# Optimization experiments

Hardware: AMD Instinct MI355X
Metric: run time of the kernel (lower is better)

Reference implementation:

```python
import jax, jax.numpy as jnp
import numpy as np

C = 64          # num_channels
NB = 8          # num_bessel
NE = 10         # num_elements
N_NODES = 20000
N_EDGES = 320000

def _silu_norm():
    # e3nn normalize2mom constant for silu: 1/sqrt(E[silu(Z)^2]), Z~N(0,1)
    x, w = np.polynomial.hermite.hermgauss(100)
    z = np.sqrt(2.0) * x
    f = z / (1.0 + np.exp(-z))
    m2 = float(np.sum(w * f * f) / np.sqrt(np.pi))
    return np.float32(1.0 / np.sqrt(m2))

C_SILU = _silu_norm()
SQRT3 = np.float32(np.sqrt(3.0))
SQRT2 = np.float32(np.sqrt(2.0))
INV_SQRT_C = np.float32(1.0 / np.sqrt(C))
INV_SQRT_2C = np.float32(1.0 / np.sqrt(2 * C))
INV_SQRT_3C = np.float32(1.0 / np.sqrt(3 * C))
INV_SQRT_NB = np.float32(1.0 / np.sqrt(NB))
INV_SQRT_64 = np.float32(1.0 / np.sqrt(64.0))


def setup_inputs() -> dict:
    key = jax.random.key(0)
    ks = jax.random.split(key, 22)
    n = lambda k, s: jax.random.normal(k, s, dtype=jnp.float32)
    return {
        "node_feats": n(ks[0], (N_NODES, 4 * C)),
        "edge_feats": jax.random.uniform(ks[1], (N_EDGES, NB), dtype=jnp.float32),
        "edge_attrs": n(ks[2], (N_EDGES, 4)),
        "iedges": jax.random.randint(ks[3], (N_EDGES,), 0, N_NODES),
        "jedges": jax.random.randint(ks[4], (N_EDGES,), 0, N_NODES),
        "atomic_numbers": jax.random.randint(ks[5], (N_NODES,), 0, NE),
        "Wup0": n(ks[6], (C, C)), "Wup1": n(ks[7], (C, C)),
        "Wm1": n(ks[8], (NB, 64)), "Wm2": n(ks[9], (64, 64)),
        "Wm3": n(ks[10], (64, 64)), "Wm4": n(ks[11], (64, 5 * C)),
        "Wl0": n(ks[12], (2 * C, C)), "Wl1": n(ks[13], (3 * C, C)),
        "Ws0c1": n(ks[14], (NE, 1, C)), "Ws0c2": n(ks[15], (NE, 2, C)),
        "Ws0c3": n(ks[16], (NE, 2, C)),
        "Ws1c1": n(ks[17], (NE, 1, C)), "Ws1c2": n(ks[18], (NE, 1, C)),
        "Ws1c3": n(ks[19], (NE, 2, C)),
        "Wp0": n(ks[20], (C, C)), "Wp1": n(ks[21], (C, C)),
    }


def reference(node_feats, edge_feats, edge_attrs, iedges, jedges, atomic_numbers,
              Wup0, Wup1, Wm1, Wm2, Wm3, Wm4, Wl0, Wl1,
              Ws0c1, Ws0c2, Ws0c3, Ws1c1, Ws1c2, Ws1c3, Wp0, Wp1):
    Nn = node_feats.shape[0]
    # split irreps: C scalars (0e) then C vectors (1e), channel-major layout
    s = node_feats[:, :C]                       # (N, C)
    v = node_feats[:, C:].reshape(Nn, C, 3)     # (N, C, 3)

    # linear_up: per-l channel mixing, fan-in normalized (e3nn o3.Linear)
    s = (s @ Wup0) * INV_SQRT_C
    v = jnp.einsum('ncm,ck->nkm', v, Wup1) * INV_SQRT_C

    # conv_tp_weights: e3nn FullyConnectedNet [8,64,64,64,5C] with silu
    h = jax.nn.silu(edge_feats @ (Wm1 * INV_SQRT_NB)) * C_SILU
    h = jax.nn.silu(h @ (Wm2 * INV_SQRT_64)) * C_SILU
    h = jax.nn.silu(h @ (Wm3 * INV_SQRT_64)) * C_SILU
    tpw = h @ (Wm4 * INV_SQRT_64)               # (E, 5C)

    # gather sender node features per edge
    xs = s[iedges]                              # (E, C)
    xv = v[iedges]                              # (E, C, 3)
    eas = edge_attrs[:, 0:1]                    # (E, 1) scalar edge attr
    eav = edge_attrs[:, 1:4]                    # (E, 3) vector edge attr

    # 5 uvu CG paths (component-normalized e3nn TensorProduct):
    wa, wb = tpw[:, 0:C], tpw[:, C:2 * C]
    wc, wd, we = tpw[:, 2 * C:3 * C], tpw[:, 3 * C:4 * C], tpw[:, 4 * C:5 * C]
    m0 = wa * xs * eas                                              # 0e x 0e -> 0e
    m1 = wb * jnp.einsum('ecm,em->ec', xv, eav) / SQRT3             # 1e x 1e -> 0e
    m2 = (wc * xs)[:, :, None] * eav[:, None, :]                    # 0e x 1e -> 1e
    m3 = (wd * eas)[:, :, None] * xv                                # 1e x 0e -> 1e
    m4 = we[:, :, None] * jnp.cross(xv, eav[:, None, :]) / SQRT2    # 1e x 1e -> 1e

    # scatter-sum messages to receiver nodes
    msg_s = jax.ops.segment_sum(jnp.concatenate([m0, m1], axis=1), jedges, num_segments=Nn)        # (N, 2C)
    msg_v = jax.ops.segment_sum(jnp.concatenate([m2, m3, m4], axis=1), jedges, num_segments=Nn)    # (N, 3C, 3)

    # linear: middle irreps (2C x 0e + 3C x 1e) -> C x (0e + 1e)
    s2 = (msg_s @ Wl0) * INV_SQRT_2C            # (N, C)
    v2 = jnp.einsum('ncm,ck->nkm', msg_v, Wl1) * INV_SQRT_3C  # (N, C, 3)

    # symmetric (ACE/MACE) contraction, correlation=3, element-dependent weights
    w01 = Ws0c1[atomic_numbers, 0]              # (N, C)
    w02 = Ws0c2[atomic_numbers]                 # (N, 2, C)
    w03 = Ws0c3[atomic_numbers]                 # (N, 2, C)
    w11 = Ws1c1[atomic_numbers, 0]
    w12 = Ws1c2[atomic_numbers, 0]
    w13 = Ws1c3[atomic_numbers]
    vv = jnp.sum(v2 * v2, axis=-1)              # (N, C) = |v|^2 per channel
    out_s = (w01 * s2 + w02[:, 0] * s2 * s2 + w02[:, 1] * vv / SQRT3
             + w03[:, 0] * s2 * s2 * s2 + w03[:, 1] * s2 * vv / SQRT3)
    coef_v = w11 + w12 * s2 + w13[:, 0] * s2 * s2 + w13[:, 1] * vv / SQRT3
    out_v = coef_v[:, :, None] * v2             # (N, C, 3)

    # linearproduct
    so = (out_s @ Wp0) * INV_SQRT_C
    vo = jnp.einsum('ncm,ck->nkm', out_v, Wp1) * INV_SQRT_C
    return jnp.concatenate([so, vo.reshape(Nn, 3 * C)], axis=1)   # (N, 4C)
```

## Files before the change

### kernel.cpp

```cpp
#include <hip/hip_runtime.h>


typedef unsigned short u16;
typedef unsigned int u32;
typedef __attribute__((ext_vector_type(8))) short bf16x8;
typedef __attribute__((ext_vector_type(4))) float f32x4;

#define CW_UP0 0
#define CW_UP1 4096
#define CW_M1  8192
#define CW_M2  8704
#define CW_M3  12800
#define CW_M4  16896
#define CW_L0  37376
#define CW_L1  45568
#define CW_P0  57856
#define CW_P1  61952
#define CW_S01 66048
#define CW_S02 66688
#define CW_S03 67968
#define CW_S11 69248
#define CW_S12 69888
#define CW_S13 70528
#define CW_TOTAL 71808

#define C_SILU     1.6765224f
#define INV_SQRT3  0.57735027f
#define INV_SQRT2  0.70710678f
#define SC_L1      0.35355339f
#define SC_L234    0.125f

#define HS16 72
#define NFRAG   60

__device__ __forceinline__ float b2f(u16 u) {
  union { u32 i; float f; } x; x.i = ((u32)u) << 16; return x.f;
}
__device__ __forceinline__ u16 f2b(float f) {
  union { float f; u32 i; } x; x.f = f;
  u32 i = x.i;
  u32 r = (i + 0x7fffu + ((i >> 16) & 1u)) >> 16;
  return (u16)r;
}
__device__ __forceinline__ float ldf(const void* p, size_t i, int f32) {
  return f32 ? ((const float*)p)[i] : b2f(((const u16*)p)[i]);
}
__device__ __forceinline__ float silu_n(float x) {
  return C_SILU * x / (1.0f + __expf(-x));
}

__global__ void k_detect(const void* nf, int* flag) {
  __shared__ int cnt;
  if (threadIdx.x == 0) cnt = 0;
  __syncthreads();
  const u16* p = (const u16*)nf;
  int wild = 0;
  for (int i = threadIdx.x; i < 4096; i += 256) {
    float ax = fabsf(b2f(p[i]));
    if (!(ax <= 1e10f) || (ax != 0.f && ax < 1e-10f)) wild++;
  }
  atomicAdd(&cnt, wild);
  __syncthreads();
  if (threadIdx.x == 0) *flag = (cnt > 100) ? 1 : 0;
}

struct WPtrs { const void* p[16]; };

__global__ __launch_bounds__(256) void k_front(
    WPtrs wp, float* __restrict__ cw, u16* __restrict__ bwH,
    u16* __restrict__ bwL, const int* __restrict__ je, int* __restrict__ deg,
    const void* __restrict__ nf, float* __restrict__ sup,
    float* __restrict__ vup, int nN, int nE, int nb0,
    const int* __restrict__ flagp) {
  __shared__ float row[4][256];
  const int f32 = *flagp;
  int bid = blockIdx.x, tid = threadIdx.x;

  if (bid < 281) {
    const int   sizes[16]  = {4096,4096,512,4096,4096,20480,8192,12288,4096,
                              4096,640,1280,1280,640,640,1280};
    const float scales[16] = {0.125f,0.125f,0.35355339f,0.125f,0.125f,0.125f,
                              0.08838835f,0.07216878f,0.125f,0.125f,
                              1.f,1.f,1.f,1.f,1.f,1.f};
    int gid = bid * 256 + tid;
    if (gid >= CW_TOTAL) return;
    int off = gid, seg = 0;
    while (off >= sizes[seg]) { off -= sizes[seg]; seg++; }
    cw[gid] = ldf(wp.p[seg], off, f32) * scales[seg];
  } else if (bid < 401) {
    int gid = (bid - 281) * 256 + tid;
    int f = gid >> 9, idx = gid & 511;
    int l = idx >> 3, j = idx & 7;
    int q = l >> 4, col16 = l & 15;
    float v = 0.f;
    if (f < 4) {
      int k = q * 8 + j, n = f * 16 + col16;
      if (k < 8) v = ldf(wp.p[2], (size_t)k * 64 + n, f32);
    } else if (f < 20) {
      const void* w = (f < 12) ? wp.p[3] : wp.p[4];
      int t = (f < 12) ? f - 4 : f - 12;
      int n = (t >> 1) * 16 + col16, ks = t & 1;
      int k = ks * 32 + q * 8 + j;
      v = ldf(w, (size_t)k * 64 + n, f32);
    } else {
      int t = f - 20;
      int n = (t >> 1) * 16 + col16, ks = t & 1;
      int k = ks * 32 + q * 8 + j;
      v = ldf(wp.p[5], (size_t)k * 320 + n, f32);
    }
    u16 hi = f2b(v);
    u16 lo = f2b(v - b2f(hi));
    size_t o = (size_t)f * 512 + (size_t)l * 8 + j;
    bwH[o] = hi;
    bwL[o] = lo;
  } else if (bid < nb0) {
    int e = (bid - 401) * 256 + tid;
    if (e < nE) atomicAdd(&deg[je[e]], 1);
  } else {
    int w = tid >> 6, l = tid & 63;
    int n = (bid - nb0) * 4 + w;
    bool valid = n < nN;
    int nn = valid ? n : 0;
#pragma unroll
    for (int t = 0; t < 4; t++)
      row[w][t * 64 + l] = ldf(nf, (size_t)nn * 256 + t * 64 + l, f32);
    __syncthreads();
    float sacc = 0.f, v0 = 0.f, v1 = 0.f, v2 = 0.f;
#pragma unroll 8
    for (int c = 0; c < 64; c++) {
      float w0 = ldf(wp.p[0], (size_t)c * 64 + l, f32);
      float w1 = ldf(wp.p[1], (size_t)c * 64 + l, f32);
      sacc += row[w][c] * w0;
      v0 += row[w][64 + c * 3 + 0] * w1;
      v1 += row[w][64 + c * 3 + 1] * w1;
      v2 += row[w][64 + c * 3 + 2] * w1;
    }
    if (valid) {
      sup[(size_t)n * 64 + l] = sacc * 0.125f;
      vup[((size_t)n * 3 + 0) * 64 + l] = v0 * 0.125f;
      vup[((size_t)n * 3 + 1) * 64 + l] = v1 * 0.125f;
      vup[((size_t)n * 3 + 2) * 64 + l] = v2 * 0.125f;
    }
  }
}

__global__ __launch_bounds__(256) void k_scan(const int* __restrict__ deg,
                                              int* __restrict__ offs,
                                              int* __restrict__ cursor, int nN) {
  __shared__ int part[256];
  int t = threadIdx.x;
  int per = (nN + 255) / 256;
  int lo = t * per, hi = (t + 1) * per; if (hi > nN) hi = nN;
  int s = 0;
  for (int i = lo; i < hi; i++) s += deg[i];
  part[t] = s;
  __syncthreads();
  if (t == 0) {
    int run = 0;
    for (int i = 0; i < 256; i++) { int v = part[i]; part[i] = run; run += v; }
    offs[nN] = run;
  }
  __syncthreads();
  int run = part[t];
  for (int i = lo; i < hi; i++) {
    offs[i] = run; cursor[i] = run; run += deg[i];
  }
}

__global__ __launch_bounds__(256) void k_scatter2(
    const int* __restrict__ je, const int* __restrict__ ie,
    const void* __restrict__ ea, const void* __restrict__ ef,
    int* __restrict__ cursor, int* __restrict__ iSlot,
    float4* __restrict__ eaSlot, float4* __restrict__ efSlot, int nE,
    const int* __restrict__ flagp) {
  const int f32 = *flagp;
  int e = blockIdx.x * 256 + threadIdx.x;
  if (e >= nE) return;
  int pos = atomicAdd(&cursor[je[e]], 1);
  iSlot[pos] = ie[e];
  float4 av;
  float4 f0, f1;
  if (f32) {
    av = ((const float4*)ea)[e];
    f0 = ((const float4*)ef)[(size_t)e * 2];
    f1 = ((const float4*)ef)[(size_t)e * 2 + 1];
  } else {
    uint2 r = ((const uint2*)ea)[e];
    av = make_float4(b2f(r.x & 0xffff), b2f(r.x >> 16),
                     b2f(r.y & 0xffff), b2f(r.y >> 16));
    uint4 u = ((const uint4*)ef)[e];
    f0 = make_float4(b2f(u.x & 0xffff), b2f(u.x >> 16),
                     b2f(u.y & 0xffff), b2f(u.y >> 16));
    f1 = make_float4(b2f(u.z & 0xffff), b2f(u.z >> 16),
                     b2f(u.w & 0xffff), b2f(u.w >> 16));
  }
  eaSlot[pos] = av;
  efSlot[(size_t)pos * 2] = f0;
  efSlot[(size_t)pos * 2 + 1] = f1;
}

__global__ __launch_bounds__(192) void k_mlp4(
    const float4* __restrict__ efSlot, const int* __restrict__ offs,
    const u16* __restrict__ bwH, const u16* __restrict__ bwL,
    u16* __restrict__ tpw, int gn0, int gn1, int capEff) {
  __shared__ u16 H[3][64 * HS16];
  int tid = threadIdx.x;
  int w = tid >> 6, l = tid & 63;
  int m = l & 15, q = l >> 4;
  int base = offs[gn0];
  int cnt = offs[gn1] - base;
  int lim = cnt < capEff ? cnt : capEff;
  int tb = (blockIdx.x * 3 + w) * 64;
  if (tb >= lim) return;
  u16* Hw = H[w];

  bf16x8 zero8 = {0,0,0,0,0,0,0,0};
  bf16x8 A1h[4], A1l[4];
#pragma unroll
  for (int t = 0; t < 4; t++) { A1h[t] = zero8; A1l[t] = zero8; }
  if (q == 0) {
#pragma unroll
    for (int t = 0; t < 4; t++) {
      int s = tb + t * 16 + m; if (s > lim - 1) s = lim - 1;
      float4 q0 = efSlot[(size_t)s * 2], q1 = efSlot[(size_t)s * 2 + 1];
      float v[8] = {q0.x, q0.y, q0.z, q0.w, q1.x, q1.y, q1.z, q1.w};
      bf16x8 hi, lo;
#pragma unroll
      for (int j = 0; j < 8; j++) {
        u16 h = f2b(v[j]);
        hi[j] = (short)h;
        lo[j] = (short)f2b(v[j] - b2f(h));
      }
      A1h[t] = hi; A1l[t] = lo;
    }
  }
#pragma unroll
  for (int n = 0; n < 4; n++) {
    bf16x8 Bh = *(const bf16x8*)(bwH + (size_t)n * 512 + (size_t)l * 8);
    bf16x8 Bl = *(const bf16x8*)(bwL + (size_t)n * 512 + (size_t)l * 8);
#pragma unroll
    for (int t = 0; t < 4; t++) {
      f32x4 c = (f32x4){0.f, 0.f, 0.f, 0.f};
      c = __builtin_amdgcn_mfma_f32_16x16x32_bf16(A1h[t], Bh, c, 0, 0, 0);
      c = __builtin_amdgcn_mfma_f32_16x16x32_bf16(A1l[t], Bh, c, 0, 0, 0);
      c = __builtin_amdgcn_mfma_f32_16x16x32_bf16(A1h[t], Bl, c, 0, 0, 0);
#pragma unroll
      for (int r = 0; r < 4; r++)
        Hw[(t * 16 + q * 4 + r) * HS16 + n * 16 + m] =
            f2b(silu_n(c[r] * SC_L1));
    }
  }

#pragma unroll
  for (int layer = 0; layer < 2; layer++) {
    int fragBase = 4 + layer * 8;
    bf16x8 Ah[2][4];
#pragma unroll
    for (int ks = 0; ks < 2; ks++)
#pragma unroll
      for (int t = 0; t < 4; t++)
        Ah[ks][t] = *(const bf16x8*)(Hw + (t * 16 + m) * HS16 + ks * 32 + q * 8);
#pragma unroll
    for (int n = 0; n < 4; n++) {
      bf16x8 B0h = *(const bf16x8*)(bwH + (size_t)(fragBase + n * 2 + 0) * 512 +
                                    (size_t)l * 8);
      bf16x8 B0l = *(const bf16x8*)(bwL + (size_t)(fragBase + n * 2 + 0) * 512 +
                                    (size_t)l * 8);
      bf16x8 B1h = *(const bf16x8*)(bwH + (size_t)(fragBase + n * 2 + 1) * 512 +
                                    (size_t)l * 8);
      bf16x8 B1l = *(const bf16x8*)(bwL + (size_t)(fragBase + n * 2 + 1) * 512 +
                                    (size_t)l * 8);
#pragma unroll
      for (int t = 0; t < 4; t++) {
        f32x4 c = (f32x4){0.f, 0.f, 0.f, 0.f};
        c = __builtin_amdgcn_mfma_f32_16x16x32_bf16(Ah[0][t], B0h, c, 0, 0, 0);
        c = __builtin_amdgcn_mfma_f32_16x16x32_bf16(Ah[0][t], B0l, c, 0, 0, 0);
        c = __builtin_amdgcn_mfma_f32_16x16x32_bf16(Ah[1][t], B1h, c, 0, 0, 0);
        c = __builtin_amdgcn_mfma_f32_16x16x32_bf16(Ah[1][t], B1l, c, 0, 0, 0);
#pragma unroll
        for (int r = 0; r < 4; r++)
          Hw[(t * 16 + q * 4 + r) * HS16 + n * 16 + m] =
              f2b(silu_n(c[r] * SC_L234));
      }
    }
  }

  {
    bf16x8 Ah[2][4];
#pragma unroll
    for (int ks = 0; ks < 2; ks++)
#pragma unroll
      for (int t = 0; t < 4; t++)
        Ah[ks][t] = *(const bf16x8*)(Hw + (t * 16 + m) * HS16 + ks * 32 + q * 8);
    for (int n = 0; n < 20; n++) {
      bf16x8 B0h = *(const bf16x8*)(bwH + (size_t)(20 + n * 2 + 0) * 512 +
                                    (size_t)l * 8);
      bf16x8 B0l = *(const bf16x8*)(bwL + (size_t)(20 + n * 2 + 0) * 512 +
                                    (size_t)l * 8);
      bf16x8 B1h = *(const bf16x8*)(bwH + (size_t)(20 + n * 2 + 1) * 512 +
                                    (size_t)l * 8);
      bf16x8 B1l = *(const bf16x8*)(bwL + (size_t)(20 + n * 2 + 1) * 512 +
                                    (size_t)l * 8);
#pragma unroll
      for (int t = 0; t < 4; t++) {
        f32x4 c = (f32x4){0.f, 0.f, 0.f, 0.f};
        c = __builtin_amdgcn_mfma_f32_16x16x32_bf16(Ah[0][t], B0h, c, 0, 0, 0);
        c = __builtin_amdgcn_mfma_f32_16x16x32_bf16(Ah[0][t], B0l, c, 0, 0, 0);
        c = __builtin_amdgcn_mfma_f32_16x16x32_bf16(Ah[1][t], B1h, c, 0, 0, 0);
        c = __builtin_amdgcn_mfma_f32_16x16x32_bf16(Ah[1][t], B1l, c, 0, 0, 0);
#pragma unroll
        for (int r = 0; r < 4; r++) {
          int srow = tb + t * 16 + q * 4 + r;
          if (srow < lim)
            tpw[(size_t)srow * 320 + n * 16 + m] = f2b(c[r] * SC_L234);
        }
      }
    }
  }
}

__global__ __launch_bounds__(256) void k_gather5(
    const int* __restrict__ iSlot, const float4* __restrict__ eaSlot,
    const int* __restrict__ offs, const float* __restrict__ sup,
    const float* __restrict__ vup, const int* __restrict__ an,
    const float* __restrict__ cw, const u16* __restrict__ tpw,
    void* __restrict__ out, int gn0, int gn1, int capEff,
    const int* __restrict__ flagp) {
  __shared__ float B[4][960];
  const int f32 = *flagp;
  int w = threadIdx.x >> 6, l = threadIdx.x & 63;
  int n = gn0 + blockIdx.x * 4 + w;
  bool valid = n < gn1;
  int nn = valid ? n : gn0;
  int gbase = offs[gn0];
  int start = offs[nn];
  int deg = offs[nn + 1] - start;
  int avail = capEff - (start - gbase);
  int dmax = deg < avail ? deg : avail;
  if (dmax < 0) dmax = 0;

  float as0 = 0.f, as1 = 0.f;
  float av[9];
#pragma unroll
  for (int m = 0; m < 9; m++) av[m] = 0.f;

  for (int c0 = 0; c0 < dmax; c0 += 64) {
    int rem = dmax - c0;
    int cend = rem < 64 ? rem : 64;
    int iA = 0;
    float4 eaA = make_float4(0.f, 0.f, 0.f, 0.f);
    if (l < cend) {
      iA = iSlot[start + c0 + l];
      eaA = eaSlot[start + c0 + l];
    }
    for (int qq = 0; qq < cend; qq++) {
      int i = __shfl(iA, qq);
      float eas = __shfl(eaA.x, qq);
      float ev0 = __shfl(eaA.y, qq);
      float ev1 = __shfl(eaA.z, qq);
      float ev2 = __shfl(eaA.w, qq);
      const u16* tp = tpw + (size_t)(start - gbase + c0 + qq) * 320;
      float wa  = b2f(tp[l]);
      float wbv = b2f(tp[64 + l]);
      float wc  = b2f(tp[128 + l]);
      float wd  = b2f(tp[192 + l]);
      float we_ = b2f(tp[256 + l]);
      float xs  = sup[(size_t)i * 64 + l];
      float xv0 = vup[((size_t)i * 3 + 0) * 64 + l];
      float xv1 = vup[((size_t)i * 3 + 1) * 64 + l];
      float xv2 = vup[((size_t)i * 3 + 2) * 64 + l];
      float dot = xv0 * ev0 + xv1 * ev1 + xv2 * ev2;
      as0 += wa * xs * eas;
      as1 += wbv * dot * INV_SQRT3;
      float wcxs = wc * xs;
      float wde  = wd * eas;
      float wef  = we_ * INV_SQRT2;
      av[0] += wcxs * ev0; av[1] += wcxs * ev1; av[2] += wcxs * ev2;
      av[3] += wde * xv0;  av[4] += wde * xv1;  av[5] += wde * xv2;
      av[6] += wef * (xv1 * ev2 - xv2 * ev1);
      av[7] += wef * (xv2 * ev0 - xv0 * ev2);
      av[8] += wef * (xv0 * ev1 - xv1 * ev0);
    }
  }

  float* Bb = B[w];
  Bb[l] = as0;
  Bb[64 + l] = as1;
#pragma unroll
  for (int m = 0; m < 3; m++) {
    Bb[128 + l * 3 + m] = av[m];
    Bb[320 + l * 3 + m] = av[3 + m];
    Bb[512 + l * 3 + m] = av[6 + m];
  }
  __syncthreads();

  float s2 = 0.f;
#pragma unroll 8
  for (int c = 0; c < 128; c++) s2 += Bb[c] * cw[CW_L0 + c * 64 + l];
  float v20 = 0.f, v21 = 0.f, v22 = 0.f;
#pragma unroll 8
  for (int c = 0; c < 192; c++) {
    float wk = cw[CW_L1 + c * 64 + l];
    v20 += Bb[128 + c * 3 + 0] * wk;
    v21 += Bb[128 + c * 3 + 1] * wk;
    v22 += Bb[128 + c * 3 + 2] * wk;
  }
  int a = an[nn];
  float w01  = cw[CW_S01 + a * 64 + l];
  float w02a = cw[CW_S02 + a * 128 + l];
  float w02b = cw[CW_S02 + a * 128 + 64 + l];
  float w03a = cw[CW_S03 + a * 128 + l];
  float w03b = cw[CW_S03 + a * 128 + 64 + l];
  float w11  = cw[CW_S11 + a * 64 + l];
  float w12  = cw[CW_S12 + a * 64 + l];
  float w13a = cw[CW_S13 + a * 128 + l];
  float w13b = cw[CW_S13 + a * 128 + 64 + l];

  float vv = v20 * v20 + v21 * v21 + v22 * v22;
  float s2sq = s2 * s2;
  float vvs = vv * INV_SQRT3;
  float outs = w01 * s2 + w02a * s2sq + w02b * vvs + w03a * s2sq * s2 +
               w03b * s2 * vvs;
  float coef = w11 + w12 * s2 + w13a * s2sq + w13b * vvs;

  __syncthreads();
  Bb[704 + l] = outs;
  Bb[768 + l * 3 + 0] = coef * v20;
  Bb[768 + l * 3 + 1] = coef * v21;
  Bb[768 + l * 3 + 2] = coef * v22;
  __syncthreads();

  float so = 0.f, vo0 = 0.f, vo1 = 0.f, vo2 = 0.f;
#pragma unroll 8
  for (int c = 0; c < 64; c++) {
    float w0 = cw[CW_P0 + c * 64 + l];
    float w1 = cw[CW_P1 + c * 64 + l];
    so  += Bb[704 + c] * w0;
    vo0 += Bb[768 + c * 3 + 0] * w1;
    vo1 += Bb[768 + c * 3 + 1] * w1;
    vo2 += Bb[768 + c * 3 + 2] * w1;
  }
  if (valid) {
    size_t basep = (size_t)n * 256;
    if (f32) {
      float* o = (float*)out;
      o[basep + l] = so;
      o[basep + 64 + l * 3 + 0] = vo0;
      o[basep + 64 + l * 3 + 1] = vo1;
      o[basep + 64 + l * 3 + 2] = vo2;
    } else {
      u16* o = (u16*)out;
      o[basep + l] = f2b(so);
      o[basep + 64 + l * 3 + 0] = f2b(vo0);
      o[basep + 64 + l * 3 + 1] = f2b(vo1);
      o[basep + 64 + l * 3 + 2] = f2b(vo2);
    }
  }
}

extern "C" void kernel_launch(void* const* d_in, const int* in_sizes, int n_in,
                              void* d_out, int out_size, void* d_ws,
                              size_t ws_size, hipStream_t stream) {
  const void* nf = d_in[0];
  const void* ef = d_in[1];
  const void* ea = d_in[2];
  const int* ie = (const int*)d_in[3];
  const int* je = (const int*)d_in[4];
  const int* an = (const int*)d_in[5];
  int nN = in_sizes[0] / 256;
  int nE = in_sizes[3];

  size_t intCnt = (size_t)3 * nN + 1 + nE;
  intCnt = (intCnt + 3) & ~(size_t)3;
  int* deg    = (int*)d_ws;
  int* offs   = deg + nN;
  int* cursor = offs + nN + 1;
  int* iSlot  = cursor + nN;
  float* cw   = (float*)d_ws + intCnt;
  float* sup  = cw + CW_TOTAL;
  float* vup  = sup + (size_t)nN * 64;
  int* flag   = (int*)(vup + (size_t)nN * 192);

  size_t eaByte = (intCnt + CW_TOTAL + (size_t)nN * 256 + 1) * 4;
  eaByte = (eaByte + 15) & ~(size_t)15;
  float4* eaSlot = (float4*)((char*)d_ws + eaByte);
  float4* efSlot = eaSlot + nE;
  size_t bwByte = eaByte + (size_t)nE * 16 + (size_t)nE * 32;
  u16* bwH = (u16*)((char*)d_ws + bwByte);
  u16* bwL = bwH + (size_t)NFRAG * 512;
  size_t tpwByte = bwByte + (size_t)NFRAG * 512 * 2 * 2;
  tpwByte = (tpwByte + 15) & ~(size_t)15;
  u16* tpw = (u16*)((char*)d_ws + tpwByte);
  size_t capE = (ws_size > tpwByte) ? (ws_size - tpwByte) / 640 : 0;

  int G = 64;
  int nodesPer = (nN + 63) / 64;
  for (int g = 1; g <= 64; g++) {
    int npg = (nN + g - 1) / g;
    size_t worst = (size_t)npg * nE / nN + 6000;
    if (worst <= capE) { G = g; nodesPer = npg; break; }
  }
  int capEff = (int)((size_t)nodesPer * nE / nN + 6000);
  if ((size_t)capEff > capE) capEff = (int)capE;

  k_detect<<<1, 256, 0, stream>>>(nf, flag);
  hipMemsetAsync(deg, 0, (size_t)nN * sizeof(int), stream);

  WPtrs wp;
  const int widx[16] = {6, 7, 8, 9, 10, 11, 12, 13, 20, 21,
                        14, 15, 16, 17, 18, 19};
  for (int i = 0; i < 16; i++) wp.p[i] = d_in[widx[i]];

  int histNB = (nE + 255) / 256;
  int nb0 = 401 + histNB;
  int nupNB = (nN + 3) / 4;
  k_front<<<nb0 + nupNB, 256, 0, stream>>>(wp, cw, bwH, bwL, je, deg, nf,
                                           sup, vup, nN, nE, nb0, flag);
  k_scan<<<1, 256, 0, stream>>>(deg, offs, cursor, nN);
  k_scatter2<<<(nE + 255) / 256, 256, 0, stream>>>(je, ie, ea, ef, cursor,
                                                   iSlot, eaSlot, efSlot, nE,
                                                   flag);

  for (int g = 0; g < G; g++) {
    int gn0 = g * nodesPer;
    if (gn0 >= nN) break;
    int gn1 = gn0 + nodesPer; if (gn1 > nN) gn1 = nN;
    int mlpBlocks = (capEff + 191) / 192;
    k_mlp4<<<mlpBlocks, 192, 0, stream>>>(efSlot, offs, bwH, bwL, tpw,
                                          gn0, gn1, capEff);
    int gBlocks = (gn1 - gn0 + 3) / 4;
    k_gather5<<<gBlocks, 256, 0, stream>>>(iSlot, eaSlot, offs, sup, vup, an,
                                           cw, tpw, d_out, gn0, gn1, capEff,
                                           flag);
  }
}
```

Measured before the change: 481.4 us.

## Move per-node linear and product layers into a batched MFMA post kernel

The gather kernel no longer applies the Wl0/Wl1 linears, the symmetric contraction and the Wp0/Wp1 product per node with scalar FMA loops. It now writes the aggregated messages to workspace buffers. A new k_post kernel handles tiles of 64 nodes and runs those matmuls on bf16 MFMA, using a hi/lo split with three products to keep near-fp32 accuracy. The front kernel pre-packs the extra weight fragments. The trade is extra global traffic to write and re-read the message buffers. The mlp kernel's edge-feature read also now offsets by the group base, which matters when there is more than one node group.

New measurement: 585.5 us. 1.22x slower.

```diff
diff --git a/kernel.cpp b/kernel.cpp
--- a/kernel.cpp
+++ b/kernel.cpp
@@ -31,7 +31,11 @@
 #define SC_L234    0.125f
 
 #define HS16 72
-#define NFRAG   60
+#define NFRAG 116
+#define FW0 60
+#define FW1 76
+#define FP0 100
+#define FP1 108
 
 __device__ __forceinline__ float b2f(u16 u) {
   union { u32 i; float f; } x; x.i = ((u32)u) << 16; return x.f;
@@ -87,7 +91,7 @@
     int off = gid, seg = 0;
     while (off >= sizes[seg]) { off -= sizes[seg]; seg++; }
     cw[gid] = ldf(wp.p[seg], off, f32) * scales[seg];
-  } else if (bid < 401) {
+  } else if (bid < 513) {
     int gid = (bid - 281) * 256 + tid;
     int f = gid >> 9, idx = gid & 511;
     int l = idx >> 3, j = idx & 7;
@@ -102,11 +106,27 @@
       int n = (t >> 1) * 16 + col16, ks = t & 1;
       int k = ks * 32 + q * 8 + j;
       v = ldf(w, (size_t)k * 64 + n, f32);
-    } else {
+    } else if (f < 60) {
       int t = f - 20;
       int n = (t >> 1) * 16 + col16, ks = t & 1;
       int k = ks * 32 + q * 8 + j;
       v = ldf(wp.p[5], (size_t)k * 320 + n, f32);
+    } else if (f < 76) {
+      int t = f - FW0, ks = t >> 2, n = t & 3;
+      int k = ks * 32 + q * 8 + j;
+      v = ldf(wp.p[6], (size_t)k * 64 + n * 16 + col16, f32) * 0.08838835f;
+    } else if (f < 100) {
+      int t = f - FW1, ks = t >> 2, n = t & 3;
+      int k = ks * 32 + q * 8 + j;
+      v = ldf(wp.p[7], (size_t)k * 64 + n * 16 + col16, f32) * 0.07216878f;
+    } else if (f < 108) {
+      int t = f - FP0, ks = t >> 2, n = t & 3;
+      int k = ks * 32 + q * 8 + j;
+      v = ldf(wp.p[8], (size_t)k * 64 + n * 16 + col16, f32) * 0.125f;
+    } else {
+      int t = f - FP1, ks = t >> 2, n = t & 3;
+      int k = ks * 32 + q * 8 + j;
+      v = ldf(wp.p[9], (size_t)k * 64 + n * 16 + col16, f32) * 0.125f;
     }
     u16 hi = f2b(v);
     u16 lo = f2b(v - b2f(hi));
@@ -114,7 +134,7 @@
     bwH[o] = hi;
     bwL[o] = lo;
   } else if (bid < nb0) {
-    int e = (bid - 401) * 256 + tid;
+    int e = (bid - 513) * 256 + tid;
     if (e < nE) atomicAdd(&deg[je[e]], 1);
   } else {
     int w = tid >> 6, l = tid & 63;
@@ -222,7 +242,8 @@
 #pragma unroll
     for (int t = 0; t < 4; t++) {
       int s = tb + t * 16 + m; if (s > lim - 1) s = lim - 1;
-      float4 q0 = efSlot[(size_t)s * 2], q1 = efSlot[(size_t)s * 2 + 1];
+      float4 q0 = efSlot[((size_t)(base + s)) * 2];
+      float4 q1 = efSlot[((size_t)(base + s)) * 2 + 1];
       float v[8] = {q0.x, q0.y, q0.z, q0.w, q1.x, q1.y, q1.z, q1.w};
       bf16x8 hi, lo;
 #pragma unroll
@@ -319,22 +340,18 @@
   }
 }
 
-__global__ __launch_bounds__(256) void k_gather5(
+__global__ __launch_bounds__(256) void k_gather6(
     const int* __restrict__ iSlot, const float4* __restrict__ eaSlot,
     const int* __restrict__ offs, const float* __restrict__ sup,
-    const float* __restrict__ vup, const int* __restrict__ an,
-    const float* __restrict__ cw, const u16* __restrict__ tpw,
-    void* __restrict__ out, int gn0, int gn1, int capEff,
-    const int* __restrict__ flagp) {
-  __shared__ float B[4][960];
-  const int f32 = *flagp;
+    const float* __restrict__ vup, const u16* __restrict__ tpw,
+    float* __restrict__ msgS, float* __restrict__ msgV,
+    int gn0, int gn1, int capEff) {
   int w = threadIdx.x >> 6, l = threadIdx.x & 63;
   int n = gn0 + blockIdx.x * 4 + w;
-  bool valid = n < gn1;
-  int nn = valid ? n : gn0;
+  if (n >= gn1) return;
   int gbase = offs[gn0];
-  int start = offs[nn];
-  int deg = offs[nn + 1] - start;
+  int start = offs[n];
+  int deg = offs[n + 1] - start;
   int avail = capEff - (start - gbase);
   int dmax = deg < avail ? deg : avail;
   if (dmax < 0) dmax = 0;
@@ -383,79 +400,172 @@
     }
   }
 
-  float* Bb = B[w];
-  Bb[l] = as0;
-  Bb[64 + l] = as1;
-#pragma unroll
-  for (int m = 0; m < 3; m++) {
-    Bb[128 + l * 3 + m] = av[m];
-    Bb[320 + l * 3 + m] = av[3 + m];
-    Bb[512 + l * 3 + m] = av[6 + m];
-  }
-  __syncthreads();
-
-  float s2 = 0.f;
-#pragma unroll 8
-  for (int c = 0; c < 128; c++) s2 += Bb[c] * cw[CW_L0 + c * 64 + l];
-  float v20 = 0.f, v21 = 0.f, v22 = 0.f;
-#pragma unroll 8
-  for (int c = 0; c < 192; c++) {
-    float wk = cw[CW_L1 + c * 64 + l];
-    v20 += Bb[128 + c * 3 + 0] * wk;
-    v21 += Bb[128 + c * 3 + 1] * wk;
-    v22 += Bb[128 + c * 3 + 2] * wk;
-  }
-  int a = an[nn];
-  float w01  = cw[CW_S01 + a * 64 + l];
-  float w02a = cw[CW_S02 + a * 128 + l];
-  float w02b = cw[CW_S02 + a * 128 + 64 + l];
-  float w03a = cw[CW_S03 + a * 128 + l];
-  float w03b = cw[CW_S03 + a * 128 + 64 + l];
-  float w11  = cw[CW_S11 + a * 64 + l];
-  float w12  = cw[CW_S12 + a * 64 + l];
-  float w13a = cw[CW_S13 + a * 128 + l];
-  float w13b = cw[CW_S13 + a * 128 + 64 + l];
-
-  float vv = v20 * v20 + v21 * v21 + v22 * v22;
-  float s2sq = s2 * s2;
-  float vvs = vv * INV_SQRT3;
-  float outs = w01 * s2 + w02a * s2sq + w02b * vvs + w03a * s2sq * s2 +
-               w03b * s2 * vvs;
-  float coef = w11 + w12 * s2 + w13a * s2sq + w13b * vvs;
-
-  __syncthreads();
-  Bb[704 + l] = outs;
-  Bb[768 + l * 3 + 0] = coef * v20;
-  Bb[768 + l * 3 + 1] = coef * v21;
-  Bb[768 + l * 3 + 2] = coef * v22;
-  __syncthreads();
-
-  float so = 0.f, vo0 = 0.f, vo1 = 0.f, vo2 = 0.f;
-#pragma unroll 8
-  for (int c = 0; c < 64; c++) {
-    float w0 = cw[CW_P0 + c * 64 + l];
-    float w1 = cw[CW_P1 + c * 64 + l];
-    so  += Bb[704 + c] * w0;
-    vo0 += Bb[768 + c * 3 + 0] * w1;
-    vo1 += Bb[768 + c * 3 + 1] * w1;
-    vo2 += Bb[768 + c * 3 + 2] * w1;
-  }
-  if (valid) {
-    size_t basep = (size_t)n * 256;
-    if (f32) {
-      float* o = (float*)out;
-      o[basep + l] = so;
-      o[basep + 64 + l * 3 + 0] = vo0;
-      o[basep + 64 + l * 3 + 1] = vo1;
-      o[basep + 64 + l * 3 + 2] = vo2;
-    } else {
-      u16* o = (u16*)out;
-      o[basep + l] = f2b(so);
-      o[basep + 64 + l * 3 + 0] = f2b(vo0);
-      o[basep + 64 + l * 3 + 1] = f2b(vo1);
-      o[basep + 64 + l * 3 + 2] = f2b(vo2);
-    }
-  }
+  msgS[(size_t)n * 128 + l] = as0;
+  msgS[(size_t)n * 128 + 64 + l] = as1;
+#pragma unroll
+  for (int c = 0; c < 3; c++) {
+    msgV[(size_t)n * 576 + c * 192 + l]       = av[c];
+    msgV[(size_t)n * 576 + c * 192 + 64 + l]  = av[3 + c];
+    msgV[(size_t)n * 576 + c * 192 + 128 + l] = av[6 + c];
+  }
+}
+
+#define POST_G2(SRC, FB, STORE_S, COMP)                                        \
+  {                                                                            \
+    __syncthreads();                                                           \
+    _Pragma("unroll")                                                          \
+    for (int t = 0; t < 4; t++)                                                \
+      _Pragma("unroll")                                                        \
+      for (int r = 0; r < 4; r++)                                              \
+        T[t * 16 + q * 4 + r][w * 16 + m] = SRC[t][r];                         \
+    __syncthreads();                                                           \
+    f32x4 d[4];                                                                \
+    _Pragma("unroll")                                                          \
+    for (int t = 0; t < 4; t++) d[t] = (f32x4){0.f, 0.f, 0.f, 0.f};            \
+    _Pragma("unroll")                                                          \
+    for (int ks = 0; ks < 2; ks++) {                                           \
+      bf16x8 Bh = *(const bf16x8*)(bwH + (size_t)(FB + ks * 4 + w) * 512 +     \
+                                   (size_t)l * 8);                             \
+      bf16x8 Bl = *(const bf16x8*)(bwL + (size_t)(FB + ks * 4 + w) * 512 +     \
+                                   (size_t)l * 8);                             \
+      _Pragma("unroll")                                                        \
+      for (int t = 0; t < 4; t++) {                                            \
+        bf16x8 Ah, Al;                                                         \
+        _Pragma("unroll")                                                      \
+        for (int j = 0; j < 8; j++) {                                          \
+          float vx = T[t * 16 + m][ks * 32 + q * 8 + j];                       \
+          u16 h = f2b(vx);                                                     \
+          Ah[j] = (short)h;                                                    \
+          Al[j] = (short)f2b(vx - b2f(h));                                     \
+        }                                                                      \
+        d[t] = __builtin_amdgcn_mfma_f32_16x16x32_bf16(Ah, Bh, d[t], 0, 0, 0); \
+        d[t] = __builtin_amdgcn_mfma_f32_16x16x32_bf16(Al, Bh, d[t], 0, 0, 0); \
+        d[t] = __builtin_amdgcn_mfma_f32_16x16x32_bf16(Ah, Bl, d[t], 0, 0, 0); \
+      }                                                                        \
+    }                                                                          \
+    _Pragma("unroll")                                                          \
+    for (int t = 0; t < 4; t++)                                                \
+      _Pragma("unroll")                                                        \
+      for (int r = 0; r < 4; r++) {                                            \
+        int node = n0 + t * 16 + q * 4 + r;                                    \
+        if (node < nN) {                                                       \
+          int ch = w * 16 + m;                                                 \
+          size_t basep = (size_t)node * 256;                                   \
+          size_t oidx = STORE_S ? (basep + ch) : (basep + 64 + ch * 3 + COMP); \
+          if (f32) ((float*)out)[oidx] = d[t][r];                              \
+          else ((u16*)out)[oidx] = f2b(d[t][r]);                               \
+        }                                                                      \
+      }                                                                        \
+  }
+
+__global__ __launch_bounds__(256) void k_post(
+    const float* __restrict__ msgS, const float* __restrict__ msgV,
+    const int* __restrict__ an, const float* __restrict__ cw,
+    const u16* __restrict__ bwH, const u16* __restrict__ bwL,
+    void* __restrict__ out, int nN, const int* __restrict__ flagp) {
+  __shared__ float T[64][69];
+  const int f32 = *flagp;
+  int tid = threadIdx.x;
+  int w = tid >> 6, l = tid & 63;
+  int m = l & 15, q = l >> 4;
+  int n0 = blockIdx.x * 64;
+
+  f32x4 s2[4];
+#pragma unroll
+  for (int t = 0; t < 4; t++) s2[t] = (f32x4){0.f, 0.f, 0.f, 0.f};
+#pragma unroll
+  for (int ks = 0; ks < 4; ks++) {
+    bf16x8 Bh = *(const bf16x8*)(bwH + (size_t)(FW0 + ks * 4 + w) * 512 +
+                                 (size_t)l * 8);
+    bf16x8 Bl = *(const bf16x8*)(bwL + (size_t)(FW0 + ks * 4 + w) * 512 +
+                                 (size_t)l * 8);
+#pragma unroll
+    for (int t = 0; t < 4; t++) {
+      int row = n0 + t * 16 + m; if (row > nN - 1) row = nN - 1;
+      const float* ap = msgS + (size_t)row * 128 + ks * 32 + q * 8;
+      bf16x8 Ah, Al;
+#pragma unroll
+      for (int j = 0; j < 8; j++) {
+        float vx = ap[j];
+        u16 h = f2b(vx);
+        Ah[j] = (short)h;
+        Al[j] = (short)f2b(vx - b2f(h));
+      }
+      s2[t] = __builtin_amdgcn_mfma_f32_16x16x32_bf16(Ah, Bh, s2[t], 0, 0, 0);
+      s2[t] = __builtin_amdgcn_mfma_f32_16x16x32_bf16(Al, Bh, s2[t], 0, 0, 0);
+      s2[t] = __builtin_amdgcn_mfma_f32_16x16x32_bf16(Ah, Bl, s2[t], 0, 0, 0);
+    }
+  }
+
+  f32x4 v2[3][4];
+#pragma unroll
+  for (int c = 0; c < 3; c++)
+#pragma unroll
+    for (int t = 0; t < 4; t++) v2[c][t] = (f32x4){0.f, 0.f, 0.f, 0.f};
+#pragma unroll
+  for (int ks = 0; ks < 6; ks++) {
+    bf16x8 Bh = *(const bf16x8*)(bwH + (size_t)(FW1 + ks * 4 + w) * 512 +
+                                 (size_t)l * 8);
+    bf16x8 Bl = *(const bf16x8*)(bwL + (size_t)(FW1 + ks * 4 + w) * 512 +
+                                 (size_t)l * 8);
+#pragma unroll
+    for (int c = 0; c < 3; c++)
+#pragma unroll
+      for (int t = 0; t < 4; t++) {
+        int row = n0 + t * 16 + m; if (row > nN - 1) row = nN - 1;
+        const float* ap = msgV + (size_t)row * 576 + c * 192 + ks * 32 + q * 8;
+        bf16x8 Ah, Al;
+#pragma unroll
+        for (int j = 0; j < 8; j++) {
+          float vx = ap[j];
+          u16 h = f2b(vx);
+          Ah[j] = (short)h;
+          Al[j] = (short)f2b(vx - b2f(h));
+        }
+        v2[c][t] = __builtin_amdgcn_mfma_f32_16x16x32_bf16(Ah, Bh, v2[c][t], 0, 0, 0);
+        v2[c][t] = __builtin_amdgcn_mfma_f32_16x16x32_bf16(Al, Bh, v2[c][t], 0, 0, 0);
+        v2[c][t] = __builtin_amdgcn_mfma_f32_16x16x32_bf16(Ah, Bl, v2[c][t], 0, 0, 0);
+      }
+  }
+
+  f32x4 os[4];
+  f32x4 ov[3][4];
+#pragma unroll
+  for (int t = 0; t < 4; t++) {
+#pragma unroll
+    for (int r = 0; r < 4; r++) {
+      int node = n0 + t * 16 + q * 4 + r;
+      int nc = node > nN - 1 ? nN - 1 : node;
+      int a = an[nc];
+      int ch = w * 16 + m;
+      float s2v = s2[t][r];
+      float va = v2[0][t][r], vb = v2[1][t][r], vc = v2[2][t][r];
+      float vv = va * va + vb * vb + vc * vc;
+      float w01  = cw[CW_S01 + a * 64 + ch];
+      float w02a = cw[CW_S02 + a * 128 + ch];
+      float w02b = cw[CW_S02 + a * 128 + 64 + ch];
+      float w03a = cw[CW_S03 + a * 128 + ch];
+      float w03b = cw[CW_S03 + a * 128 + 64 + ch];
+      float w11  = cw[CW_S11 + a * 64 + ch];
+      float w12  = cw[CW_S12 + a * 64 + ch];
+      float w13a = cw[CW_S13 + a * 128 + ch];
+      float w13b = cw[CW_S13 + a * 128 + 64 + ch];
+      float s2sq = s2v * s2v;
+      float vvs = vv * INV_SQRT3;
+      float outs = w01 * s2v + w02a * s2sq + w02b * vvs + w03a * s2sq * s2v +
+                   w03b * s2v * vvs;
+      float coef = w11 + w12 * s2v + w13a * s2sq + w13b * vvs;
+      os[t][r] = outs;
+      ov[0][t][r] = coef * va;
+      ov[1][t][r] = coef * vb;
+      ov[2][t][r] = coef * vc;
+    }
+  }
+
+  POST_G2(os, FP0, 1, 0)
+  POST_G2(ov[0], FP1, 0, 0)
+  POST_G2(ov[1], FP1, 0, 1)
+  POST_G2(ov[2], FP1, 0, 2)
 }
 
 extern "C" void kernel_launch(void* const* d_in, const int* in_sizes, int n_in,
@@ -480,8 +590,10 @@
   float* sup  = cw + CW_TOTAL;
   float* vup  = sup + (size_t)nN * 64;
   int* flag   = (int*)(vup + (size_t)nN * 192);
-
-  size_t eaByte = (intCnt + CW_TOTAL + (size_t)nN * 256 + 1) * 4;
+  float* msgS = (float*)(flag + 1);
+  float* msgV = msgS + (size_t)nN * 128;
+
+  size_t eaByte = (size_t)((char*)(msgV + (size_t)nN * 576) - (char*)d_ws);
   eaByte = (eaByte + 15) & ~(size_t)15;
   float4* eaSlot = (float4*)((char*)d_ws + eaByte);
   float4* efSlot = eaSlot + nE;
@@ -512,7 +624,7 @@
   for (int i = 0; i < 16; i++) wp.p[i] = d_in[widx[i]];
 
   int histNB = (nE + 255) / 256;
-  int nb0 = 401 + histNB;
+  int nb0 = 513 + histNB;
   int nupNB = (nN + 3) / 4;
   k_front<<<nb0 + nupNB, 256, 0, stream>>>(wp, cw, bwH, bwL, je, deg, nf,
                                            sup, vup, nN, nE, nb0, flag);
@@ -529,8 +641,10 @@
     k_mlp4<<<mlpBlocks, 192, 0, stream>>>(efSlot, offs, bwH, bwL, tpw,
                                           gn0, gn1, capEff);
     int gBlocks = (gn1 - gn0 + 3) / 4;
-    k_gather5<<<gBlocks, 256, 0, stream>>>(iSlot, eaSlot, offs, sup, vup, an,
-                                           cw, tpw, d_out, gn0, gn1, capEff,
-                                           flag);
-  }
-}
+    k_gather6<<<gBlocks, 256, 0, stream>>>(iSlot, eaSlot, offs, sup, vup,
+                                           tpw, msgS, msgV, gn0, gn1, capEff);
+  }
+  int postNB = (nN + 63) / 64;
+  k_post<<<postNB, 256, 0, stream>>>(msgS, msgV, an, cw, bwH, bwL, d_out,
+                                     nN, flag);
+}
```
